# Performance work log

Measured on AMD Instinct MI355X. Metric: run time of the kernel, lower is better.

Reference implementation:

```python
import jax, jax.numpy as jnp
import numpy as np

B, C, H, W = 4, 64, 64, 64

def setup_inputs() -> dict:
    key = jax.random.key(0)
    ks = jax.random.split(key, 8)
    s = 1.0 / np.sqrt(C)
    return {
        "x": jax.random.normal(ks[0], (B, C, H, W), dtype=jnp.float32),
        "Wq": jax.random.normal(ks[1], (C, C), dtype=jnp.float32) * s,
        "bq": jax.random.normal(ks[2], (C,), dtype=jnp.float32) * s,
        "Wk": jax.random.normal(ks[3], (C, C), dtype=jnp.float32) * s,
        "bk": jax.random.normal(ks[4], (C,), dtype=jnp.float32) * s,
        "Wv": jax.random.normal(ks[5], (C, C), dtype=jnp.float32) * s,
        "bv": jax.random.normal(ks[6], (C,), dtype=jnp.float32) * s,
        "gamma": jax.random.normal(ks[7], (1,), dtype=jnp.float32),
    }

def reference(x, Wq, bq, Wk, bk, Wv, bv, gamma):
    b, c, h, w = x.shape
    xf = x.reshape(b, c, h * w)                      # [B, C, N]
    q = jnp.einsum('oc,bcn->bon', Wq, xf) + bq[None, :, None]
    k = jnp.einsum('oc,bcn->bon', Wk, xf) + bk[None, :, None]
    v = jnp.einsum('oc,bcn->bon', Wv, xf) + bv[None, :, None]
    energy = jnp.einsum('bci,bcj->bij', q, k)        # [B, N, N] = Q^T K
    attn = jax.nn.softmax(energy, axis=-1)
    # out[b,c,i] = sum_j v[b,c,j] * attn[b,i,j]
    out = jnp.einsum('bcj,bij->bci', v, attn)        # [B, C, N]
    out = out.reshape(b, c, h, w)
    return gamma[0] * out + x
```

## Files before the change

kernel.cpp:

```cpp
#include <hip/hip_runtime.h>
#include <hip/hip_bf16.h>
#include <math.h>


constexpr int C_ = 64;
constexpr int N_ = 4096;
constexpr float LOG2E = 1.4426950408889634f;
constexpr float MBIAS = 86.5617f;

typedef float  f4 __attribute__((ext_vector_type(4)));
typedef short  s8 __attribute__((ext_vector_type(8)));

__device__ inline unsigned short f2bf(float x) {
    union { float f; unsigned u; } a; a.f = x;
    unsigned r = a.u + 0x7FFFu + ((a.u >> 16) & 1u);
    return (unsigned short)(r >> 16);
}
__device__ inline float bf2f(unsigned short h) {
    union { float f; unsigned u; } a; a.u = ((unsigned)h) << 16; return a.f;
}
__device__ inline uint4 pack8(const float* v) {
    uint4 r;
    r.x = (unsigned)f2bf(v[0]) | ((unsigned)f2bf(v[1]) << 16);
    r.y = (unsigned)f2bf(v[2]) | ((unsigned)f2bf(v[3]) << 16);
    r.z = (unsigned)f2bf(v[4]) | ((unsigned)f2bf(v[5]) << 16);
    r.w = (unsigned)f2bf(v[6]) | ((unsigned)f2bf(v[7]) << 16);
    return r;
}
__device__ inline void pack8_split(const float* v, uint4* hi, uint4* lo) {
    unsigned short h[8]; float rem[8];
    #pragma unroll
    for (int i = 0; i < 8; ++i) { h[i] = f2bf(v[i]); rem[i] = v[i] - bf2f(h[i]); }
    hi->x = (unsigned)h[0] | ((unsigned)h[1] << 16);
    hi->y = (unsigned)h[2] | ((unsigned)h[3] << 16);
    hi->z = (unsigned)h[4] | ((unsigned)h[5] << 16);
    hi->w = (unsigned)h[6] | ((unsigned)h[7] << 16);
    *lo = pack8(rem);
}

__global__ __launch_bounds__(256) void prep_kernel(
    const float* __restrict__ x,
    const float* __restrict__ Wq, const float* __restrict__ bq,
    const float* __restrict__ Wk, const float* __restrict__ bk,
    const float* __restrict__ Wv, const float* __restrict__ bv,
    unsigned short* __restrict__ qhi, unsigned short* __restrict__ qlo,
    unsigned short* __restrict__ khi, unsigned short* __restrict__ klo,
    unsigned short* __restrict__ vv)
{
    __shared__ __align__(16) char smem[62208];
    float (*xs)[36]  = (float(*)[36])(smem);
    float (*wqs)[68] = (float(*)[68])(smem + 9216);
    float (*wks)[68] = (float(*)[68])(smem + 26624);
    float (*wvs)[68] = (float(*)[68])(smem + 44032);
    float* bias      = (float*)(smem + 61440);

    const int t    = threadIdx.x;
    const int nt2  = blockIdx.x, b = blockIdx.y;
    const int n0   = nt2 * 32;
    const int nt64 = nt2 >> 1, joff = (nt2 & 1) * 32;

    {
        const int nl = t & 31, cb = t >> 5;
        #pragma unroll
        for (int it = 0; it < 8; ++it) {
            int c = it * 8 + cb;
            xs[c][nl] = x[((long)b * 64 + c) * N_ + n0 + nl];
        }
        #pragma unroll
        for (int kk = 0; kk < 4; ++kk) {
            int f = t * 4 + kk * 1024;
            int o = f >> 6, c = f & 63;
            float4 w = *(const float4*)&Wq[f];
            wqs[c+0][o] = w.x; wqs[c+1][o] = w.y; wqs[c+2][o] = w.z; wqs[c+3][o] = w.w;
            w = *(const float4*)&Wk[f];
            wks[c+0][o] = w.x; wks[c+1][o] = w.y; wks[c+2][o] = w.z; wks[c+3][o] = w.w;
            w = *(const float4*)&Wv[f];
            wvs[c+0][o] = w.x; wvs[c+1][o] = w.y; wvs[c+2][o] = w.z; wvs[c+3][o] = w.w;
        }
        if (t < 64) { bias[t] = bq[t]; bias[64 + t] = bk[t]; bias[128 + t] = bv[t]; }
    }
    __syncthreads();

    const int o4 = (t & 15) * 4, n2 = (t >> 4) * 2;
    float aq[4][2], ak[4][2], av[4][2];
    #pragma unroll
    for (int oo = 0; oo < 4; ++oo) {
        aq[oo][0] = bias[o4 + oo];        aq[oo][1] = aq[oo][0];
        ak[oo][0] = bias[64 + o4 + oo];   ak[oo][1] = ak[oo][0];
        av[oo][0] = bias[128 + o4 + oo];  av[oo][1] = av[oo][0];
    }
    #pragma unroll 4
    for (int c = 0; c < 64; ++c) {
        float2 xv = *(const float2*)&xs[c][n2];
        f4 w1 = *(const f4*)&wqs[c][o4];
        f4 w2 = *(const f4*)&wks[c][o4];
        f4 w3 = *(const f4*)&wvs[c][o4];
        #pragma unroll
        for (int oo = 0; oo < 4; ++oo) {
            aq[oo][0] = fmaf(w1[oo], xv.x, aq[oo][0]);
            aq[oo][1] = fmaf(w1[oo], xv.y, aq[oo][1]);
            ak[oo][0] = fmaf(w2[oo], xv.x, ak[oo][0]);
            ak[oo][1] = fmaf(w2[oo], xv.y, ak[oo][1]);
            av[oo][0] = fmaf(w3[oo], xv.x, av[oo][0]);
            av[oo][1] = fmaf(w3[oo], xv.y, av[oo][1]);
        }
    }
    __syncthreads();

    {
        float (*qst)[68] = wqs;
        float (*kst)[68] = wks;
        float (*vst)[36] = xs;
        #pragma unroll
        for (int oo = 0; oo < 4; ++oo) {
            qst[n2][o4 + oo]     = aq[oo][0] * LOG2E;
            qst[n2 + 1][o4 + oo] = aq[oo][1] * LOG2E;
            kst[n2][o4 + oo]     = ak[oo][0];
            kst[n2 + 1][o4 + oo] = ak[oo][1];
            vst[o4 + oo][n2]     = av[oo][0];
            vst[o4 + oo][n2 + 1] = av[oo][1];
        }
    }
    __syncthreads();

    const long gbase = ((long)b * 64 + nt64) * 512;
    float tmp[8];
    {
        float (*qst)[68] = wqs;
        int mloc = t >> 7, ks = (t >> 6) & 1, L = t & 63;
        int m = (joff >> 4) + mloc;
        int rowl = mloc * 16 + (L & 15), c0 = ks * 32 + ((L >> 4) & 3) * 8;
        *(f4*)tmp       = *(const f4*)&qst[rowl][c0];
        *(f4*)(tmp + 4) = *(const f4*)&qst[rowl][c0 + 4];
        uint4 hi, lo; pack8_split(tmp, &hi, &lo);
        long ch = gbase + (m * 2 + ks) * 64 + L;
        *(uint4*)(qhi + ch * 8) = hi;
        *(uint4*)(qlo + ch * 8) = lo;
    }
    {
        float (*kst)[68] = wks;
        int cc = t >> 5, jl = t & 31;
        *(f4*)tmp       = *(const f4*)&kst[jl][cc * 8];
        *(f4*)(tmp + 4) = *(const f4*)&kst[jl][cc * 8 + 4];
        uint4 hi, lo; pack8_split(tmp, &hi, &lo);
        long ch = gbase + cc * 64 + joff + jl;
        *(uint4*)(khi + ch * 8) = hi;
        *(uint4*)(klo + ch * 8) = lo;
    }
    {
        float (*vst)[36] = xs;
        int cj = t >> 6, c = t & 63;
        *(f4*)tmp       = *(const f4*)&vst[c][cj * 8];
        *(f4*)(tmp + 4) = *(const f4*)&vst[c][cj * 8 + 4];
        long ch = gbase + ((joff >> 3) + cj) * 64 + c;
        *(uint4*)(vv + ch * 8) = pack8(tmp);
    }
}

__global__ __launch_bounds__(256, 4) void attn_kernel(
    const unsigned short* __restrict__ qhi, const unsigned short* __restrict__ qlo,
    const unsigned short* __restrict__ khi, const unsigned short* __restrict__ klo,
    const unsigned short* __restrict__ vv,
    float* __restrict__ Opart, float* __restrict__ lpart,
    int njt, int Bn)
{
    __shared__ __align__(16) char pst_all[4 * 4608];

    const int t  = threadIdx.x;
    const int w  = t >> 6, L = t & 63;
    char* pst = pst_all + w * 4608;
    const int lh = L >> 4, ll = L & 15;
    const int ib2 = blockIdx.x * 4 + w;
    const int ib  = ib2 >> 1, mo = (ib2 & 1) * 2;
    const int jc = blockIdx.y, b = blockIdx.z;

    s8 qh[2][2], ql[2][2];
    {
        const int qb = (b * 64 + ib) * 512;
        #pragma unroll
        for (int m = 0; m < 2; ++m)
            #pragma unroll
            for (int ks = 0; ks < 2; ++ks) {
                int ch = qb + ((mo + m) * 2 + ks) * 64 + L;
                qh[m][ks] = *(const s8*)(qhi + (long)ch * 8);
                ql[m][ks] = *(const s8*)(qlo + (long)ch * 8);
            }
    }

    f4 O[2][4];
    #pragma unroll
    for (int m = 0; m < 2; ++m)
        #pragma unroll
        for (int nn = 0; nn < 4; ++nn) O[m][nn] = (f4){0.f, 0.f, 0.f, 0.f};
    float lp[2][4];
    #pragma unroll
    for (int m = 0; m < 2; ++m)
        #pragma unroll
        for (int r = 0; r < 4; ++r) lp[m][r] = 0.f;

    const int jt0 = jc * njt;
    for (int jt = 0; jt < njt; ++jt) {
        const int kb = (b * 64 + jt0 + jt) * 512;

        #pragma unroll
        for (int js = 0; js < 4; ++js) {
            __builtin_amdgcn_sched_barrier(0);
            s8 bh[2], bl[2];
            #pragma unroll
            for (int ks = 0; ks < 2; ++ks) {
                int ch = kb + (ks * 4 + lh) * 64 + js * 16 + ll;
                bh[ks] = *(const s8*)(khi + (long)ch * 8);
                bl[ks] = *(const s8*)(klo + (long)ch * 8);
            }
            #pragma unroll
            for (int m = 0; m < 2; ++m) {
                f4 acc = (f4){0.f, 0.f, 0.f, 0.f};
                acc = __builtin_amdgcn_mfma_f32_16x16x32_bf16(qh[m][0], bh[0], acc, 0, 0, 0);
                acc = __builtin_amdgcn_mfma_f32_16x16x32_bf16(qh[m][1], bh[1], acc, 0, 0, 0);
                acc = __builtin_amdgcn_mfma_f32_16x16x32_bf16(qh[m][0], bl[0], acc, 0, 0, 0);
                acc = __builtin_amdgcn_mfma_f32_16x16x32_bf16(qh[m][1], bl[1], acc, 0, 0, 0);
                acc = __builtin_amdgcn_mfma_f32_16x16x32_bf16(ql[m][0], bh[0], acc, 0, 0, 0);
                acc = __builtin_amdgcn_mfma_f32_16x16x32_bf16(ql[m][1], bh[1], acc, 0, 0, 0);
                #pragma unroll
                for (int r = 0; r < 4; ++r) {
                    float p = __builtin_amdgcn_exp2f(acc[r] - MBIAS);
                    lp[m][r] += p;
                    int row = m * 16 + lh * 4 + r;
                    int col = js * 16 + ll;
                    *(unsigned short*)(pst + row * 144 + col * 2) = f2bf(p);
                }
            }
        }
        __builtin_amdgcn_sched_barrier(0);

        #pragma unroll
        for (int ks = 0; ks < 2; ++ks) {
            s8 bvf[4];
            #pragma unroll
            for (int nn = 0; nn < 4; ++nn) {
                int ch = kb + (ks * 4 + lh) * 64 + nn * 16 + ll;
                bvf[nn] = *(const s8*)(vv + (long)ch * 8);
            }
            #pragma unroll
            for (int m = 0; m < 2; ++m) {
                s8 ap = *(const s8*)(pst + (m * 16 + ll) * 144 + ks * 64 + lh * 16);
                #pragma unroll
                for (int nn = 0; nn < 4; ++nn)
                    O[m][nn] = __builtin_amdgcn_mfma_f32_16x16x32_bf16(ap, bvf[nn], O[m][nn], 0, 0, 0);
            }
        }
    }

    #pragma unroll
    for (int m = 0; m < 2; ++m)
        #pragma unroll
        for (int r = 0; r < 4; ++r) {
            float s = lp[m][r];
            s += __shfl_xor(s, 1); s += __shfl_xor(s, 2);
            s += __shfl_xor(s, 4); s += __shfl_xor(s, 8);
            lp[m][r] = s;
        }
    const long obase = ((long)jc * Bn + b) * 128 + ib2;
    if (ll == 0) {
        #pragma unroll
        for (int m = 0; m < 2; ++m)
            #pragma unroll
            for (int r = 0; r < 4; ++r)
                lpart[obase * 32 + m * 16 + lh * 4 + r] = lp[m][r];
    }
    float* op = Opart + obase * 2048;
    #pragma unroll
    for (int m = 0; m < 2; ++m)
        #pragma unroll
        for (int nn = 0; nn < 4; ++nn)
            #pragma unroll
            for (int r = 0; r < 4; ++r)
                op[(((m * 4 + nn) * 4 + r) << 6) + L] = O[m][nn][r];
}

__global__ __launch_bounds__(512) void combine_kernel(
    const float* __restrict__ Opart, const float* __restrict__ lpart,
    const float* __restrict__ x, const float* __restrict__ gamma_p,
    float* __restrict__ out, int js, int Bn)
{
    __shared__ float trn[64][36];
    __shared__ float lsc[32];
    const int t   = threadIdx.x;
    const int ib2 = blockIdx.x, b = blockIdx.y;
    const float g = gamma_p[0];

    f4 acc = (f4){0.f, 0.f, 0.f, 0.f};
    for (int jc = 0; jc < js; ++jc) {
        const float* base = Opart + (((long)jc * Bn + b) * 128 + ib2) * 2048;
        acc += *(const f4*)(base + t * 4);
    }
    if (t < 32) {
        float ls = 0.f;
        for (int jc = 0; jc < js; ++jc)
            ls += lpart[(((long)jc * Bn + b) * 128 + ib2) * 32 + t];
        lsc[t] = g / ls;
    }
    #pragma unroll
    for (int e = 0; e < 4; ++e) {
        int flat = t * 4 + e;
        int L = flat & 63, idx = flat >> 6;
        int r = idx & 3, nn = (idx >> 2) & 3, m = idx >> 4;
        int row = m * 16 + (L >> 4) * 4 + r, col = nn * 16 + (L & 15);
        trn[col][row] = acc[e];
    }
    __syncthreads();

    const int cl = t >> 3, nq = (t & 7) * 4;
    const long ob = ((long)b * 64 + cl) * N_ + ib2 * 32 + nq;
    float4 xr = *(const float4*)&x[ob];
    float4 rr;
    rr.x = trn[cl][nq + 0] * lsc[nq + 0] + xr.x;
    rr.y = trn[cl][nq + 1] * lsc[nq + 1] + xr.y;
    rr.z = trn[cl][nq + 2] * lsc[nq + 2] + xr.z;
    rr.w = trn[cl][nq + 3] * lsc[nq + 3] + xr.w;
    *(float4*)&out[ob] = rr;
}

extern "C" void kernel_launch(void* const* d_in, const int* in_sizes, int n_in,
                              void* d_out, int out_size, void* d_ws, size_t ws_size,
                              hipStream_t stream) {
    const float* x  = (const float*)d_in[0];
    const float* Wq = (const float*)d_in[1];
    const float* bq = (const float*)d_in[2];
    const float* Wk = (const float*)d_in[3];
    const float* bk = (const float*)d_in[4];
    const float* Wv = (const float*)d_in[5];
    const float* bv = (const float*)d_in[6];
    const float* gm = (const float*)d_in[7];
    float* out = (float*)d_out;

    const int B = in_sizes[0] / (C_ * N_);
    const size_t per = (size_t)B * N_ * C_;
    char* w = (char*)d_ws;
    unsigned short* qhi = (unsigned short*)w;
    unsigned short* qlo = qhi + per;
    unsigned short* khi = qlo + per;
    unsigned short* klo = khi + per;
    unsigned short* vv  = klo + per;
    size_t base = 5 * per * sizeof(unsigned short);

    int js = 8;
    while (js > 1) {
        size_t need = base + (size_t)js *
            ((size_t)B * 128 * 2048 * 4 + (size_t)B * 128 * 32 * 4);
        if (need <= ws_size) break;
        js >>= 1;
    }
    float* Opart = (float*)(w + base);
    float* lpart = (float*)(w + base + (size_t)js * (size_t)B * 128 * 2048 * 4);

    prep_kernel<<<dim3(128, B), 256, 0, stream>>>(x, Wq, bq, Wk, bk, Wv, bv,
                                                  qhi, qlo, khi, klo, vv);
    attn_kernel<<<dim3(32, js, B), 256, 0, stream>>>(qhi, qlo, khi, klo, vv,
                                                     Opart, lpart, 64 / js, B);
    combine_kernel<<<dim3(128, B), 512, 0, stream>>>(Opart, lpart, x, gm, out, js, B);
}
```

Baseline: 137.0 us.

## Halve per-wave query rows in attention and read weights directly in prep

Each attention wave now processes 16 query rows instead of 32, so the grid doubles and the P staging buffer halves. Occupancy hint rises from 4 to 5 blocks. The combine kernel is resized to match. The prep kernel stops staging transposed weights and biases in LDS and reads them from global/L1 in 4-column chunks, which cuts shared memory from about 62KB to 26KB. The trade-off is that K/V tiles are reloaded twice as often per query row, and weight reads become uncoalesced global loads.

```diff
diff --git a/kernel.cpp b/kernel.cpp
--- a/kernel.cpp
+++ b/kernel.cpp
@@ -47,12 +47,11 @@
     unsigned short* __restrict__ khi, unsigned short* __restrict__ klo,
     unsigned short* __restrict__ vv)
 {
-    __shared__ __align__(16) char smem[62208];
+    __shared__ __align__(16) char smem[26624];
     float (*xs)[36]  = (float(*)[36])(smem);
-    float (*wqs)[68] = (float(*)[68])(smem + 9216);
-    float (*wks)[68] = (float(*)[68])(smem + 26624);
-    float (*wvs)[68] = (float(*)[68])(smem + 44032);
-    float* bias      = (float*)(smem + 61440);
+    float (*qst)[68] = (float(*)[68])(smem + 9216);
+    float (*kst)[68] = (float(*)[68])(smem + 17920);
+    float (*vst)[36] = (float(*)[36])(smem);
 
     const int t    = threadIdx.x;
     const int nt2  = blockIdx.x, b = blockIdx.y;
@@ -66,18 +65,6 @@
             int c = it * 8 + cb;
             xs[c][nl] = x[((long)b * 64 + c) * N_ + n0 + nl];
         }
-        #pragma unroll
-        for (int kk = 0; kk < 4; ++kk) {
-            int f = t * 4 + kk * 1024;
-            int o = f >> 6, c = f & 63;
-            float4 w = *(const float4*)&Wq[f];
-            wqs[c+0][o] = w.x; wqs[c+1][o] = w.y; wqs[c+2][o] = w.z; wqs[c+3][o] = w.w;
-            w = *(const float4*)&Wk[f];
-            wks[c+0][o] = w.x; wks[c+1][o] = w.y; wks[c+2][o] = w.z; wks[c+3][o] = w.w;
-            w = *(const float4*)&Wv[f];
-            wvs[c+0][o] = w.x; wvs[c+1][o] = w.y; wvs[c+2][o] = w.z; wvs[c+3][o] = w.w;
-        }
-        if (t < 64) { bias[t] = bq[t]; bias[64 + t] = bk[t]; bias[128 + t] = bv[t]; }
     }
     __syncthreads();
 
@@ -85,48 +72,49 @@
     float aq[4][2], ak[4][2], av[4][2];
     #pragma unroll
     for (int oo = 0; oo < 4; ++oo) {
-        aq[oo][0] = bias[o4 + oo];        aq[oo][1] = aq[oo][0];
-        ak[oo][0] = bias[64 + o4 + oo];   ak[oo][1] = ak[oo][0];
-        av[oo][0] = bias[128 + o4 + oo];  av[oo][1] = av[oo][0];
-    }
-    #pragma unroll 4
-    for (int c = 0; c < 64; ++c) {
-        float2 xv = *(const float2*)&xs[c][n2];
-        f4 w1 = *(const f4*)&wqs[c][o4];
-        f4 w2 = *(const f4*)&wks[c][o4];
-        f4 w3 = *(const f4*)&wvs[c][o4];
+        aq[oo][0] = bq[o4 + oo]; aq[oo][1] = aq[oo][0];
+        ak[oo][0] = bk[o4 + oo]; ak[oo][1] = ak[oo][0];
+        av[oo][0] = bv[o4 + oo]; av[oo][1] = av[oo][0];
+    }
+    #pragma unroll 2
+    for (int cc = 0; cc < 16; ++cc) {
+        f4 w1[4], w2[4], w3[4];
         #pragma unroll
         for (int oo = 0; oo < 4; ++oo) {
-            aq[oo][0] = fmaf(w1[oo], xv.x, aq[oo][0]);
-            aq[oo][1] = fmaf(w1[oo], xv.y, aq[oo][1]);
-            ak[oo][0] = fmaf(w2[oo], xv.x, ak[oo][0]);
-            ak[oo][1] = fmaf(w2[oo], xv.y, ak[oo][1]);
-            av[oo][0] = fmaf(w3[oo], xv.x, av[oo][0]);
-            av[oo][1] = fmaf(w3[oo], xv.y, av[oo][1]);
+            w1[oo] = *(const f4*)&Wq[(o4 + oo) * 64 + cc * 4];
+            w2[oo] = *(const f4*)&Wk[(o4 + oo) * 64 + cc * 4];
+            w3[oo] = *(const f4*)&Wv[(o4 + oo) * 64 + cc * 4];
+        }
+        #pragma unroll
+        for (int i = 0; i < 4; ++i) {
+            float2 xv = *(const float2*)&xs[cc * 4 + i][n2];
+            #pragma unroll
+            for (int oo = 0; oo < 4; ++oo) {
+                aq[oo][0] = fmaf(w1[oo][i], xv.x, aq[oo][0]);
+                aq[oo][1] = fmaf(w1[oo][i], xv.y, aq[oo][1]);
+                ak[oo][0] = fmaf(w2[oo][i], xv.x, ak[oo][0]);
+                ak[oo][1] = fmaf(w2[oo][i], xv.y, ak[oo][1]);
+                av[oo][0] = fmaf(w3[oo][i], xv.x, av[oo][0]);
+                av[oo][1] = fmaf(w3[oo][i], xv.y, av[oo][1]);
+            }
         }
     }
     __syncthreads();
 
-    {
-        float (*qst)[68] = wqs;
-        float (*kst)[68] = wks;
-        float (*vst)[36] = xs;
-        #pragma unroll
-        for (int oo = 0; oo < 4; ++oo) {
-            qst[n2][o4 + oo]     = aq[oo][0] * LOG2E;
-            qst[n2 + 1][o4 + oo] = aq[oo][1] * LOG2E;
-            kst[n2][o4 + oo]     = ak[oo][0];
-            kst[n2 + 1][o4 + oo] = ak[oo][1];
-            vst[o4 + oo][n2]     = av[oo][0];
-            vst[o4 + oo][n2 + 1] = av[oo][1];
-        }
+    #pragma unroll
+    for (int oo = 0; oo < 4; ++oo) {
+        qst[n2][o4 + oo]     = aq[oo][0] * LOG2E;
+        qst[n2 + 1][o4 + oo] = aq[oo][1] * LOG2E;
+        kst[n2][o4 + oo]     = ak[oo][0];
+        kst[n2 + 1][o4 + oo] = ak[oo][1];
+        vst[o4 + oo][n2]     = av[oo][0];
+        vst[o4 + oo][n2 + 1] = av[oo][1];
     }
     __syncthreads();
 
     const long gbase = ((long)b * 64 + nt64) * 512;
     float tmp[8];
     {
-        float (*qst)[68] = wqs;
         int mloc = t >> 7, ks = (t >> 6) & 1, L = t & 63;
         int m = (joff >> 4) + mloc;
         int rowl = mloc * 16 + (L & 15), c0 = ks * 32 + ((L >> 4) & 3) * 8;
@@ -138,7 +126,6 @@
         *(uint4*)(qlo + ch * 8) = lo;
     }
     {
-        float (*kst)[68] = wks;
         int cc = t >> 5, jl = t & 31;
         *(f4*)tmp       = *(const f4*)&kst[jl][cc * 8];
         *(f4*)(tmp + 4) = *(const f4*)&kst[jl][cc * 8 + 4];
@@ -148,7 +135,6 @@
         *(uint4*)(klo + ch * 8) = lo;
     }
     {
-        float (*vst)[36] = xs;
         int cj = t >> 6, c = t & 63;
         *(f4*)tmp       = *(const f4*)&vst[c][cj * 8];
         *(f4*)(tmp + 4) = *(const f4*)&vst[c][cj * 8 + 4];
@@ -157,46 +143,40 @@
     }
 }
 
-__global__ __launch_bounds__(256, 4) void attn_kernel(
+__global__ __launch_bounds__(256, 5) void attn_kernel(
     const unsigned short* __restrict__ qhi, const unsigned short* __restrict__ qlo,
     const unsigned short* __restrict__ khi, const unsigned short* __restrict__ klo,
     const unsigned short* __restrict__ vv,
     float* __restrict__ Opart, float* __restrict__ lpart,
     int njt, int Bn)
 {
-    __shared__ __align__(16) char pst_all[4 * 4608];
+    __shared__ __align__(16) char pst_all[4 * 2304];
 
     const int t  = threadIdx.x;
     const int w  = t >> 6, L = t & 63;
-    char* pst = pst_all + w * 4608;
+    char* pst = pst_all + w * 2304;
     const int lh = L >> 4, ll = L & 15;
-    const int ib2 = blockIdx.x * 4 + w;
-    const int ib  = ib2 >> 1, mo = (ib2 & 1) * 2;
+    const int ib16 = blockIdx.x * 4 + w;
+    const int nt64 = ib16 >> 2, mq = ib16 & 3;
     const int jc = blockIdx.y, b = blockIdx.z;
 
-    s8 qh[2][2], ql[2][2];
-    {
-        const int qb = (b * 64 + ib) * 512;
-        #pragma unroll
-        for (int m = 0; m < 2; ++m)
-            #pragma unroll
-            for (int ks = 0; ks < 2; ++ks) {
-                int ch = qb + ((mo + m) * 2 + ks) * 64 + L;
-                qh[m][ks] = *(const s8*)(qhi + (long)ch * 8);
-                ql[m][ks] = *(const s8*)(qlo + (long)ch * 8);
-            }
-    }
-
-    f4 O[2][4];
-    #pragma unroll
-    for (int m = 0; m < 2; ++m)
-        #pragma unroll
-        for (int nn = 0; nn < 4; ++nn) O[m][nn] = (f4){0.f, 0.f, 0.f, 0.f};
-    float lp[2][4];
-    #pragma unroll
-    for (int m = 0; m < 2; ++m)
-        #pragma unroll
-        for (int r = 0; r < 4; ++r) lp[m][r] = 0.f;
+    s8 qh[2], ql[2];
+    {
+        const int qb = (b * 64 + nt64) * 512;
+        #pragma unroll
+        for (int ks = 0; ks < 2; ++ks) {
+            int ch = qb + (mq * 2 + ks) * 64 + L;
+            qh[ks] = *(const s8*)(qhi + (long)ch * 8);
+            ql[ks] = *(const s8*)(qlo + (long)ch * 8);
+        }
+    }
+
+    f4 O[4];
+    #pragma unroll
+    for (int nn = 0; nn < 4; ++nn) O[nn] = (f4){0.f, 0.f, 0.f, 0.f};
+    float lp[4];
+    #pragma unroll
+    for (int r = 0; r < 4; ++r) lp[r] = 0.f;
 
     const int jt0 = jc * njt;
     for (int jt = 0; jt < njt; ++jt) {
@@ -212,23 +192,20 @@
                 bh[ks] = *(const s8*)(khi + (long)ch * 8);
                 bl[ks] = *(const s8*)(klo + (long)ch * 8);
             }
-            #pragma unroll
-            for (int m = 0; m < 2; ++m) {
-                f4 acc = (f4){0.f, 0.f, 0.f, 0.f};
-                acc = __builtin_amdgcn_mfma_f32_16x16x32_bf16(qh[m][0], bh[0], acc, 0, 0, 0);
-                acc = __builtin_amdgcn_mfma_f32_16x16x32_bf16(qh[m][1], bh[1], acc, 0, 0, 0);
-                acc = __builtin_amdgcn_mfma_f32_16x16x32_bf16(qh[m][0], bl[0], acc, 0, 0, 0);
-                acc = __builtin_amdgcn_mfma_f32_16x16x32_bf16(qh[m][1], bl[1], acc, 0, 0, 0);
-                acc = __builtin_amdgcn_mfma_f32_16x16x32_bf16(ql[m][0], bh[0], acc, 0, 0, 0);
-                acc = __builtin_amdgcn_mfma_f32_16x16x32_bf16(ql[m][1], bh[1], acc, 0, 0, 0);
-                #pragma unroll
-                for (int r = 0; r < 4; ++r) {
-                    float p = __builtin_amdgcn_exp2f(acc[r] - MBIAS);
-                    lp[m][r] += p;
-                    int row = m * 16 + lh * 4 + r;
-                    int col = js * 16 + ll;
-                    *(unsigned short*)(pst + row * 144 + col * 2) = f2bf(p);
-                }
+            f4 acc = (f4){0.f, 0.f, 0.f, 0.f};
+            acc = __builtin_amdgcn_mfma_f32_16x16x32_bf16(qh[0], bh[0], acc, 0, 0, 0);
+            acc = __builtin_amdgcn_mfma_f32_16x16x32_bf16(qh[1], bh[1], acc, 0, 0, 0);
+            acc = __builtin_amdgcn_mfma_f32_16x16x32_bf16(qh[0], bl[0], acc, 0, 0, 0);
+            acc = __builtin_amdgcn_mfma_f32_16x16x32_bf16(qh[1], bl[1], acc, 0, 0, 0);
+            acc = __builtin_amdgcn_mfma_f32_16x16x32_bf16(ql[0], bh[0], acc, 0, 0, 0);
+            acc = __builtin_amdgcn_mfma_f32_16x16x32_bf16(ql[1], bh[1], acc, 0, 0, 0);
+            #pragma unroll
+            for (int r = 0; r < 4; ++r) {
+                float p = __builtin_amdgcn_exp2f(acc[r] - MBIAS);
+                lp[r] += p;
+                int row = lh * 4 + r;
+                int col = js * 16 + ll;
+                *(unsigned short*)(pst + row * 144 + col * 2) = f2bf(p);
             }
         }
         __builtin_amdgcn_sched_barrier(0);
@@ -241,77 +218,68 @@
                 int ch = kb + (ks * 4 + lh) * 64 + nn * 16 + ll;
                 bvf[nn] = *(const s8*)(vv + (long)ch * 8);
             }
-            #pragma unroll
-            for (int m = 0; m < 2; ++m) {
-                s8 ap = *(const s8*)(pst + (m * 16 + ll) * 144 + ks * 64 + lh * 16);
-                #pragma unroll
-                for (int nn = 0; nn < 4; ++nn)
-                    O[m][nn] = __builtin_amdgcn_mfma_f32_16x16x32_bf16(ap, bvf[nn], O[m][nn], 0, 0, 0);
-            }
-        }
-    }
-
-    #pragma unroll
-    for (int m = 0; m < 2; ++m)
-        #pragma unroll
-        for (int r = 0; r < 4; ++r) {
-            float s = lp[m][r];
-            s += __shfl_xor(s, 1); s += __shfl_xor(s, 2);
-            s += __shfl_xor(s, 4); s += __shfl_xor(s, 8);
-            lp[m][r] = s;
-        }
-    const long obase = ((long)jc * Bn + b) * 128 + ib2;
+            s8 ap = *(const s8*)(pst + ll * 144 + ks * 64 + lh * 16);
+            #pragma unroll
+            for (int nn = 0; nn < 4; ++nn)
+                O[nn] = __builtin_amdgcn_mfma_f32_16x16x32_bf16(ap, bvf[nn], O[nn], 0, 0, 0);
+        }
+    }
+
+    #pragma unroll
+    for (int r = 0; r < 4; ++r) {
+        float s = lp[r];
+        s += __shfl_xor(s, 1); s += __shfl_xor(s, 2);
+        s += __shfl_xor(s, 4); s += __shfl_xor(s, 8);
+        lp[r] = s;
+    }
+    const long obase = ((long)jc * Bn + b) * 256 + ib16;
     if (ll == 0) {
         #pragma unroll
-        for (int m = 0; m < 2; ++m)
-            #pragma unroll
-            for (int r = 0; r < 4; ++r)
-                lpart[obase * 32 + m * 16 + lh * 4 + r] = lp[m][r];
-    }
-    float* op = Opart + obase * 2048;
-    #pragma unroll
-    for (int m = 0; m < 2; ++m)
-        #pragma unroll
-        for (int nn = 0; nn < 4; ++nn)
-            #pragma unroll
-            for (int r = 0; r < 4; ++r)
-                op[(((m * 4 + nn) * 4 + r) << 6) + L] = O[m][nn][r];
-}
-
-__global__ __launch_bounds__(512) void combine_kernel(
+        for (int r = 0; r < 4; ++r)
+            lpart[obase * 16 + lh * 4 + r] = lp[r];
+    }
+    float* op = Opart + obase * 1024;
+    #pragma unroll
+    for (int nn = 0; nn < 4; ++nn)
+        #pragma unroll
+        for (int r = 0; r < 4; ++r)
+            op[((nn * 4 + r) << 6) + L] = O[nn][r];
+}
+
+__global__ __launch_bounds__(256) void combine_kernel(
     const float* __restrict__ Opart, const float* __restrict__ lpart,
     const float* __restrict__ x, const float* __restrict__ gamma_p,
     float* __restrict__ out, int js, int Bn)
 {
-    __shared__ float trn[64][36];
-    __shared__ float lsc[32];
-    const int t   = threadIdx.x;
-    const int ib2 = blockIdx.x, b = blockIdx.y;
-    const float g = gamma_p[0];
+    __shared__ float trn[64][20];
+    __shared__ float lsc[16];
+    const int t    = threadIdx.x;
+    const int ib16 = blockIdx.x, b = blockIdx.y;
+    const float g  = gamma_p[0];
 
     f4 acc = (f4){0.f, 0.f, 0.f, 0.f};
     for (int jc = 0; jc < js; ++jc) {
-        const float* base = Opart + (((long)jc * Bn + b) * 128 + ib2) * 2048;
+        const float* base = Opart + (((long)jc * Bn + b) * 256 + ib16) * 1024;
         acc += *(const f4*)(base + t * 4);
     }
-    if (t < 32) {
+    if (t < 16) {
         float ls = 0.f;
         for (int jc = 0; jc < js; ++jc)
-            ls += lpart[(((long)jc * Bn + b) * 128 + ib2) * 32 + t];
+            ls += lpart[(((long)jc * Bn + b) * 256 + ib16) * 16 + t];
         lsc[t] = g / ls;
     }
     #pragma unroll
     for (int e = 0; e < 4; ++e) {
         int flat = t * 4 + e;
         int L = flat & 63, idx = flat >> 6;
-        int r = idx & 3, nn = (idx >> 2) & 3, m = idx >> 4;
-        int row = m * 16 + (L >> 4) * 4 + r, col = nn * 16 + (L & 15);
+        int r = idx & 3, nn = idx >> 2;
+        int row = (L >> 4) * 4 + r, col = nn * 16 + (L & 15);
         trn[col][row] = acc[e];
     }
     __syncthreads();
 
-    const int cl = t >> 3, nq = (t & 7) * 4;
-    const long ob = ((long)b * 64 + cl) * N_ + ib2 * 32 + nq;
+    const int cl = t >> 2, nq = (t & 3) * 4;
+    const long ob = ((long)b * 64 + cl) * N_ + ib16 * 16 + nq;
     float4 xr = *(const float4*)&x[ob];
     float4 rr;
     rr.x = trn[cl][nq + 0] * lsc[nq + 0] + xr.x;
@@ -347,16 +315,16 @@
     int js = 8;
     while (js > 1) {
         size_t need = base + (size_t)js *
-            ((size_t)B * 128 * 2048 * 4 + (size_t)B * 128 * 32 * 4);
+            ((size_t)B * 256 * 1024 * 4 + (size_t)B * 256 * 16 * 4);
         if (need <= ws_size) break;
         js >>= 1;
     }
     float* Opart = (float*)(w + base);
-    float* lpart = (float*)(w + base + (size_t)js * (size_t)B * 128 * 2048 * 4);
+    float* lpart = (float*)(w + base + (size_t)js * (size_t)B * 256 * 1024 * 4);
 
     prep_kernel<<<dim3(128, B), 256, 0, stream>>>(x, Wq, bq, Wk, bk, Wv, bv,
                                                   qhi, qlo, khi, klo, vv);
-    attn_kernel<<<dim3(32, js, B), 256, 0, stream>>>(qhi, qlo, khi, klo, vv,
+    attn_kernel<<<dim3(64, js, B), 256, 0, stream>>>(qhi, qlo, khi, klo, vv,
                                                      Opart, lpart, 64 / js, B);
-    combine_kernel<<<dim3(128, B), 512, 0, stream>>>(Opart, lpart, x, gm, out, js, B);
-}
+    combine_kernel<<<dim3(256, B), 256, 0, stream>>>(Opart, lpart, x, gm, out, js, B);
+}
```

Result: slower. 193.0 us (+40.9%).
